# Optimization experiments

Measured on AMD Instinct MI355X. Metric: run time of the kernel, lower is better.

The kernel has to match this reference:

```python
import jax, jax.numpy as jnp
import numpy as np
from jax import lax

# module constants (match init_kwargs)
CHUNK_LENGTH = 32
RIGHT_CONTEXT_LENGTH = 8
CHANNELS = 512
KERNEL_SIZE = 31
CACHE_SIZE = KERNEL_SIZE - 1  # 30


def _conv1d(x, w, b, groups=1):
    # x: (N, C_in, L), w: (C_out, C_in/groups, K), b: (C_out,)
    y = lax.conv_general_dilated(
        x, w, window_strides=(1,), padding='VALID',
        dimension_numbers=('NCH', 'OIH', 'NCH'),
        feature_group_count=groups)
    return y + b[None, :, None]


def setup_inputs() -> dict:
    key = jax.random.key(0)
    ks = jax.random.split(key, 9)
    U, B, D, R = 2048, 16, CHANNELS, 512
    s = 0.02
    return {
        'utterance': jax.random.normal(ks[0], (U, B, D), jnp.float32),
        'right_context': jax.random.normal(ks[1], (R, B, D), jnp.float32),
        'cache': jnp.zeros((B, D, CACHE_SIZE), jnp.float32),
        'w1': jax.random.normal(ks[2], (2 * D, D, 1), jnp.float32) * s,
        'b1': jax.random.normal(ks[3], (2 * D,), jnp.float32) * s,
        'wd': jax.random.normal(ks[4], (D, 1, KERNEL_SIZE), jnp.float32) * s,
        'bd': jax.random.normal(ks[5], (D,), jnp.float32) * s,
        'w2': jax.random.normal(ks[6], (D, D, 1), jnp.float32) * s,
        'b2': jax.random.normal(ks[7], (D,), jnp.float32) * s,
    }


def reference(utterance, right_context, cache, w1, b1, wd, bd, w2, b2):
    U, B, D = utterance.shape
    R = right_context.shape[0]
    rcl, cl, cs = RIGHT_CONTEXT_LENGTH, CHUNK_LENGTH, CACHE_SIZE

    # concat [right_context; utterance] along time, to (B, D, R+U)
    x = jnp.concatenate([right_context, utterance], axis=0).transpose(1, 2, 0)
    # pointwise_conv1 (ScaledConv1d == plain conv in forward math) + GLU
    # (ActivationBalancer is identity in forward)
    x = _conv1d(x, w1, b1)  # (B, 2D, R+U)
    a, g = jnp.split(x, 2, axis=1)
    x = a * jax.nn.sigmoid(g)  # GLU -> (B, D, R+U)

    utt = x[:, :, R:]      # (B, D, U)
    rc = x[:, :, :R]       # (B, D, R)

    # causal depthwise conv with left cache
    pad_utt = jnp.concatenate([cache, utt], axis=2)  # (B, D, cs+U)
    new_cache = pad_utt[:, :, -cs:]
    utt = _conv1d(pad_utt, wd, bd, groups=D)  # (B, D, U)

    # _split_right_context: gather per-chunk left cache for each rc segment
    U_ = cs + U
    num_chunks = R // rcl
    pad_utt_t = pad_utt.transpose(2, 0, 1)   # (U_, B, D)
    rc_t = rc.transpose(2, 0, 1)             # (R, B, D)
    end_idx = jnp.minimum(U_, cs + (jnp.arange(num_chunks) + 1) * cl)
    start_idx = end_idx - cs                 # (num_chunks,)
    gidx = start_idx[:, None] + jnp.arange(cs)[None, :]   # (nc, cs)
    padding = pad_utt_t[gidx]                # (nc, cs, B, D)
    padding = padding.transpose(0, 2, 1, 3).reshape(num_chunks * B, cs, D)
    rc_seg = rc_t.reshape(num_chunks, rcl, B, D).transpose(0, 2, 1, 3)
    rc_seg = rc_seg.reshape(num_chunks * B, rcl, D)
    pad_rc = jnp.concatenate([padding, rc_seg], axis=1).transpose(0, 2, 1)  # (nc*B, D, cs+rcl)
    rc_out = _conv1d(pad_rc, wd, bd, groups=D)  # (nc*B, D, rcl)
    # _merge_right_context
    rc_out = rc_out.reshape(num_chunks, B, D, rcl).transpose(1, 2, 0, 3)
    rc_out = rc_out.reshape(B, D, R)

    x = jnp.concatenate([rc_out, utt], axis=2)  # (B, D, R+U)
    # DoubleSwish: x * sigmoid(x - 1)
    x = x * jax.nn.sigmoid(x - 1.0)
    x = _conv1d(x, w2, b2)  # pointwise_conv2

    rc_final = x[:, :, :R].transpose(2, 0, 1)   # (R, B, D)
    utt_final = x[:, :, R:].transpose(2, 0, 1)  # (U, B, D)
    return utt_final, rc_final, new_cache
```

## Files before the change

### kernel.cpp

```cpp
#include <hip/hip_runtime.h>
#include <math.h>

#define B_SZ 16
#define D_CH 512
#define U_LEN 2048
#define R_LEN 512
#define T_LEN 2560
#define KS 31
#define CS 30

typedef __attribute__((ext_vector_type(8))) short short8;
typedef __attribute__((ext_vector_type(4))) float floatx4;

__device__ __forceinline__ float bf2f(ushort u) {
    unsigned v = (unsigned)u << 16;
    float f; __builtin_memcpy(&f, &v, 4); return f;
}
__device__ __forceinline__ ushort f2bf(float f) {
    unsigned v; __builtin_memcpy(&v, &f, 4);
    v += 0x7fff + ((v >> 16) & 1);
    return (ushort)(v >> 16);
}
__device__ __forceinline__ float sigmoidf_(float x) { return 1.0f / (1.0f + __expf(-x)); }

__device__ __forceinline__ void gld16(const void* g, void* l) {
    __builtin_amdgcn_global_load_lds((const __attribute__((address_space(1))) void*)g,
                                     (__attribute__((address_space(3))) void*)l, 16, 0, 0);
}

__global__ __launch_bounds__(256) void k_conv_all(
    const float* __restrict__ utt, const float* __restrict__ rc, const float* __restrict__ cache,
    const float* __restrict__ w1, const float* __restrict__ w2,
    ushort* __restrict__ xb, ushort* __restrict__ w1b, ushort* __restrict__ w2b,
    ushort* __restrict__ xc)
{
    int blk = blockIdx.x;
    if (blk < 5120) {
        size_t f4 = (size_t)blk * 1024 + threadIdx.x * 4;
        size_t o = f4 * 4;
        int q = (int)(o >> 9), d = (int)(o & 511);
        const float* src = (q < 8192) ? rc + ((size_t)q << 9) + d
                                      : utt + (((size_t)(q - 8192)) << 9) + d;
        ushort* dst = xb + o;
        #pragma unroll
        for (int i = 0; i < 4; ++i) {
            float4 v = ((const float4*)src)[i];
            ushort4 u4; u4.x = f2bf(v.x); u4.y = f2bf(v.y); u4.z = f2bf(v.z); u4.w = f2bf(v.w);
            ((ushort4*)dst)[i] = u4;
        }
    } else if (blk < 5312) {
        int t = (blk - 5120) * 1024 + threadIdx.x * 4;
        const float* src; ushort* dst;
        if (t < 131072) { src = w1; dst = w1b; }
        else            { t -= 131072; src = w2; dst = w2b; }
        #pragma unroll
        for (int i = 0; i < 4; ++i) {
            float4 v = ((const float4*)src)[t + i];
            ushort4 u4; u4.x = f2bf(v.x); u4.y = f2bf(v.y); u4.z = f2bf(v.z); u4.w = f2bf(v.w);
            ((ushort4*)dst)[t + i] = u4;
        }
    } else {
        int o = (blk - 5312) * 256 + threadIdx.x;
        int d = o & 511, p = o >> 13, b = (o >> 9) & 15;
        xc[o] = f2bf(cache[((size_t)b * D_CH + d) * CS + p]);
    }
}

__global__ __launch_bounds__(256) void k1_mfma(
    const ushort* __restrict__ xb, const ushort* __restrict__ w1b,
    const float* __restrict__ b1, ushort* __restrict__ y)
{
    __shared__ __attribute__((aligned(16))) ushort sA[2][256 * 32];
    __shared__ __attribute__((aligned(16))) ushort sBa[2][64 * 32];
    __shared__ __attribute__((aligned(16))) ushort sBg[2][64 * 32];
    const int tid = threadIdx.x;
    const int w = tid >> 6, lane = tid & 63;
    const int f = blockIdx.x;
    const int xcd = f & 7, nn = (f >> 3) & 7, qh = f >> 6;
    const int q0 = (qh * 8 + xcd) * 256;
    const int n0 = nn * 64;
    const int col = lane & 15, quad = lane >> 4;

    floatx4 acc_a[4][4], acc_g[4][4];
    #pragma unroll
    for (int i = 0; i < 4; ++i)
        #pragma unroll
        for (int j = 0; j < 4; ++j) { acc_a[i][j] = 0.f; acc_g[i][j] = 0.f; }

    const int sBs = w * 64 + lane;
    const int sBr = sBs >> 2, sBh = sBs & 3;

#define STAGE1(kc, buf) do { \
        _Pragma("unroll") \
        for (int jj = 0; jj < 4; ++jj) { \
            int s = (w * 4 + jj) * 64 + lane; \
            gld16(xb + (((size_t)(q0 + (s >> 2))) << 9) + (kc) + (s & 3) * 8, \
                  &sA[buf][(w * 4 + jj) * 512]); \
        } \
        gld16(w1b + (((size_t)(n0 + sBr)) << 9) + (kc) + sBh * 8, &sBa[buf][w * 512]); \
        gld16(w1b + (((size_t)(512 + n0 + sBr)) << 9) + (kc) + sBh * 8, &sBg[buf][w * 512]); \
    } while (0)

    STAGE1(0, 0);
    #pragma unroll
    for (int kc = 0; kc < 512; kc += 32) {
        const int buf = (kc >> 5) & 1;
        __syncthreads();
        if (kc + 32 < 512) STAGE1(kc + 32, buf ^ 1);

        short8 af[4], ba[4], bg[4];
        #pragma unroll
        for (int i = 0; i < 4; ++i)
            af[i] = *(const short8*)&sA[buf][(w * 64 + i * 16 + col) * 32 + quad * 8];
        #pragma unroll
        for (int j = 0; j < 4; ++j) {
            ba[j] = *(const short8*)&sBa[buf][(j * 16 + col) * 32 + quad * 8];
            bg[j] = *(const short8*)&sBg[buf][(j * 16 + col) * 32 + quad * 8];
        }
        #pragma unroll
        for (int i = 0; i < 4; ++i)
            #pragma unroll
            for (int j = 0; j < 4; ++j) {
                acc_a[i][j] = __builtin_amdgcn_mfma_f32_16x16x32_bf16(af[i], ba[j], acc_a[i][j], 0, 0, 0);
                acc_g[i][j] = __builtin_amdgcn_mfma_f32_16x16x32_bf16(af[i], bg[j], acc_g[i][j], 0, 0, 0);
            }
    }
#undef STAGE1

    #pragma unroll
    for (int j = 0; j < 4; ++j) {
        float bia = b1[n0 + j * 16 + col];
        float big = b1[512 + n0 + j * 16 + col];
        #pragma unroll
        for (int i = 0; i < 4; ++i) {
            #pragma unroll
            for (int r = 0; r < 4; ++r) {
                int row = q0 + w * 64 + i * 16 + quad * 4 + r;
                float a = acc_a[i][j][r] + bia;
                float g = acc_g[i][j][r] + big;
                y[((size_t)row << 9) + n0 + j * 16 + col] = f2bf(a * sigmoidf_(g));
            }
        }
    }
}

__global__ __launch_bounds__(256) void k2_fused(
    const ushort* __restrict__ y, const ushort* __restrict__ xc,
    const float* __restrict__ wd, const float* __restrict__ bd,
    ushort* __restrict__ z, float* __restrict__ out)
{
    __shared__ __attribute__((aligned(16))) char smem[20352];
    const int tid = threadIdx.x;
    int g = blockIdx.x;

    if (g < 4096) {
        ushort* sy = (ushort*)smem;
        float*  sw = (float*)(smem + 12416);
        const int u0 = (g & 31) * 64;
        const int d0 = ((g >> 5) & 7) * 64;
        const int b  = g >> 8;

        for (int idx = tid; idx < 94 * 8; idx += 256) {
            int r  = idx >> 3;
            int c8 = idx & 7;
            int p  = u0 + r;
            int dg = d0 + c8 * 8;
            const ushort* src = (p < CS) ? xc + (((size_t)(p * 16 + b)) << 9) + dg
                                         : y  + (((size_t)((482 + p) * 16 + b)) << 9) + dg;
            ushort tmp[8];
            *(int4*)tmp = *(const int4*)src;
            #pragma unroll
            for (int j = 0; j < 8; ++j) sy[(c8 * 8 + j) * 97 + r] = tmp[j];
        }
        for (int idx = tid; idx < 64 * 31; idx += 256) {
            int d = idx / 31, k = idx - d * 31;
            sw[d * 31 + k] = wd[(size_t)(d0 + d) * KS + k];
        }
        __syncthreads();

        const int dl   = tid & 63;
        const int useg = (tid >> 6) * 16;
        float win[46];
        #pragma unroll
        for (int p = 0; p < 46; ++p) win[p] = bf2f(sy[dl * 97 + useg + p]);
        float bias = bd[d0 + dl];
        float acc[16];
        #pragma unroll
        for (int i = 0; i < 16; ++i) acc[i] = bias;
        for (int k = 0; k < 31; ++k) {
            float w = sw[dl * 31 + k];
            #pragma unroll
            for (int i = 0; i < 16; ++i) acc[i] = fmaf(w, win[k + i], acc[i]);
        }
        #pragma unroll
        for (int i = 0; i < 16; ++i) {
            float v = acc[i];
            v = v * sigmoidf_(v - 1.0f);
            int u = u0 + useg + i;
            z[(((size_t)((R_LEN + u) * 16 + b)) << 9) + d0 + dl] = f2bf(v);
        }
        if ((g & 31) == 31) {
            for (int idx = tid; idx < 64 * 30; idx += 256) {
                int dl2 = idx & 63, j = idx >> 6;
                out[(size_t)20971520 + ((size_t)b * D_CH + d0 + dl2) * CS + j] = bf2f(sy[dl2 * 97 + 64 + j]);
            }
        }
    } else {
        g -= 4096;
        ushort* sy = (ushort*)smem;
        const int i  = g & 63;
        const int b  = (g >> 6) & 15;
        const int dbase = (g >> 10) * 256;

        for (int idx = tid; idx < 38 * 32; idx += 256) {
            int r  = idx >> 5;
            int c8 = idx & 31;
            int t = (r < CS) ? (R_LEN + 32 * i + 2 + r) : (8 * i + (r - CS));
            *(int4*)&sy[r * 256 + c8 * 8] =
                *(const int4*)(y + (((size_t)(t * 16 + b)) << 9) + dbase + c8 * 8);
        }
        __syncthreads();

        const int dd = dbase + tid;
        float wr[31];
        #pragma unroll
        for (int k = 0; k < 31; ++k) wr[k] = wd[(size_t)dd * KS + k];
        float bias = bd[dd];
        #pragma unroll
        for (int j = 0; j < 8; ++j) {
            float acc = bias;
            #pragma unroll
            for (int k = 0; k < 31; ++k) acc = fmaf(wr[k], bf2f(sy[(j + k) * 256 + tid]), acc);
            float v = acc * sigmoidf_(acc - 1.0f);
            z[(((size_t)((i * 8 + j) * 16 + b)) << 9) + dd] = f2bf(v);
        }
    }
}

__global__ __launch_bounds__(256) void k3_mfma(
    const ushort* __restrict__ zb, const ushort* __restrict__ w2b,
    const float* __restrict__ b2, float* __restrict__ out)
{
    __shared__ __attribute__((aligned(16))) ushort sA[2][256 * 32];
    __shared__ __attribute__((aligned(16))) ushort sB[2][64 * 32];
    const int tid = threadIdx.x;
    const int w = tid >> 6, lane = tid & 63;
    const int f = blockIdx.x;
    const int xcd = f & 7, nn = (f >> 3) & 7, qh = f >> 6;
    const int q0 = (qh * 8 + xcd) * 256;
    const int n0 = nn * 64;
    const int col = lane & 15, quad = lane >> 4;

    floatx4 acc[4][4];
    #pragma unroll
    for (int i = 0; i < 4; ++i)
        #pragma unroll
        for (int j = 0; j < 4; ++j) acc[i][j] = 0.f;

    const int sBs = w * 64 + lane;
    const int sBr = sBs >> 2, sBh = sBs & 3;

#define STAGE3(kc, buf) do { \
        _Pragma("unroll") \
        for (int jj = 0; jj < 4; ++jj) { \
            int s = (w * 4 + jj) * 64 + lane; \
            gld16(zb + (((size_t)(q0 + (s >> 2))) << 9) + (kc) + (s & 3) * 8, \
                  &sA[buf][(w * 4 + jj) * 512]); \
        } \
        gld16(w2b + (((size_t)(n0 + sBr)) << 9) + (kc) + sBh * 8, &sB[buf][w * 512]); \
    } while (0)

    STAGE3(0, 0);
    #pragma unroll
    for (int kc = 0; kc < 512; kc += 32) {
        const int buf = (kc >> 5) & 1;
        __syncthreads();
        if (kc + 32 < 512) STAGE3(kc + 32, buf ^ 1);

        short8 af[4], bf[4];
        #pragma unroll
        for (int i = 0; i < 4; ++i)
            af[i] = *(const short8*)&sA[buf][(w * 64 + i * 16 + col) * 32 + quad * 8];
        #pragma unroll
        for (int j = 0; j < 4; ++j)
            bf[j] = *(const short8*)&sB[buf][(j * 16 + col) * 32 + quad * 8];
        #pragma unroll
        for (int i = 0; i < 4; ++i)
            #pragma unroll
            for (int j = 0; j < 4; ++j)
                acc[i][j] = __builtin_amdgcn_mfma_f32_16x16x32_bf16(af[i], bf[j], acc[i][j], 0, 0, 0);
    }
#undef STAGE3

    #pragma unroll
    for (int j = 0; j < 4; ++j) {
        float bb = b2[n0 + j * 16 + col];
        #pragma unroll
        for (int i = 0; i < 4; ++i) {
            #pragma unroll
            for (int r = 0; r < 4; ++r) {
                int q = q0 + w * 64 + i * 16 + quad * 4 + r;
                float v = acc[i][j][r] + bb;
                size_t off = (q < 8192) ? (size_t)16777216 + ((size_t)q << 9)
                                        : ((size_t)(q - 8192) << 9);
                out[off + n0 + j * 16 + col] = v;
            }
        }
    }
}

extern "C" void kernel_launch(void* const* d_in, const int* in_sizes, int n_in,
                              void* d_out, int out_size, void* d_ws, size_t ws_size,
                              hipStream_t stream)
{
    const float* utt   = (const float*)d_in[0];
    const float* rc    = (const float*)d_in[1];
    const float* cache = (const float*)d_in[2];
    const float* w1    = (const float*)d_in[3];
    const float* b1    = (const float*)d_in[4];
    const float* wd    = (const float*)d_in[5];
    const float* bd    = (const float*)d_in[6];
    const float* w2    = (const float*)d_in[7];
    const float* b2    = (const float*)d_in[8];
    float* out = (float*)d_out;

    ushort* xb  = (ushort*)d_ws;
    ushort* y   = xb  + (size_t)20971520;
    ushort* zb  = y   + (size_t)20971520;
    ushort* w1b = zb  + (size_t)20971520;
    ushort* w2b = w1b + (size_t)524288;
    ushort* xc  = w2b + (size_t)262144;

    k_conv_all<<<dim3(6272), 256, 0, stream>>>(utt, rc, cache, w1, w2, xb, w1b, w2b, xc);
    k1_mfma   <<<dim3(1280), 256, 0, stream>>>(xb, w1b, b1, y);
    k2_fused  <<<dim3(6144), 256, 0, stream>>>(y, xc, wd, bd, zb, out);
    k3_mfma   <<<dim3(1280), 256, 0, stream>>>(zb, w2b, b2, out);
}
```

Before: 354.1 us.

## Retile pointwise GEMMs to 128x128 with 4-stage swizzled LDS pipeline

Both MFMA GEMM kernels switch from a 256x64 tile to a 128x128 tile with a 2x2 wave layout. LDS goes from double to quad buffering, with manual vmcnt waits and an XOR swizzle to avoid bank conflicts. MFMA sections run at raised wave priority. For the first GEMM, the w1 rows are interleaved at conversion time so each 16-column fragment pair holds matching GLU value and gate columns, letting one accumulator set cover both and letting the epilogue pair them. The aim is better operand reuse, deeper latency hiding and two blocks per CU, at the cost of relying on hand-written wait counts.

```diff
diff --git a/kernel.cpp b/kernel.cpp
--- a/kernel.cpp
+++ b/kernel.cpp
@@ -50,14 +50,25 @@
         }
     } else if (blk < 5312) {
         int t = (blk - 5120) * 1024 + threadIdx.x * 4;
-        const float* src; ushort* dst;
-        if (t < 131072) { src = w1; dst = w1b; }
-        else            { t -= 131072; src = w2; dst = w2b; }
-        #pragma unroll
-        for (int i = 0; i < 4; ++i) {
-            float4 v = ((const float4*)src)[t + i];
-            ushort4 u4; u4.x = f2bf(v.x); u4.y = f2bf(v.y); u4.z = f2bf(v.z); u4.w = f2bf(v.w);
-            ((ushort4*)dst)[t + i] = u4;
+        if (t < 131072) {
+            #pragma unroll
+            for (int i = 0; i < 4; ++i) {
+                int e = (t + i) << 2;
+                int row = e >> 9, k = e & 511;
+                int rr = row & 511;
+                int rp = (rr >> 4) * 32 + ((row >> 9) << 4) + (rr & 15);
+                float4 v = ((const float4*)w1)[t + i];
+                ushort4 u4; u4.x = f2bf(v.x); u4.y = f2bf(v.y); u4.z = f2bf(v.z); u4.w = f2bf(v.w);
+                ((ushort4*)w1b)[rp * 128 + (k >> 2)] = u4;
+            }
+        } else {
+            int t2 = t - 131072;
+            #pragma unroll
+            for (int i = 0; i < 4; ++i) {
+                float4 v = ((const float4*)w2)[t2 + i];
+                ushort4 u4; u4.x = f2bf(v.x); u4.y = f2bf(v.y); u4.z = f2bf(v.z); u4.w = f2bf(v.w);
+                ((ushort4*)w2b)[t2 + i] = u4;
+            }
         }
     } else {
         int o = (blk - 5312) * 256 + threadIdx.x;
@@ -66,79 +77,88 @@
     }
 }
 
-__global__ __launch_bounds__(256) void k1_mfma(
-    const ushort* __restrict__ xb, const ushort* __restrict__ w1b,
+__global__ __launch_bounds__(256, 2) void k1_mfma(
+    const ushort* __restrict__ xb, const ushort* __restrict__ w1p,
     const float* __restrict__ b1, ushort* __restrict__ y)
 {
-    __shared__ __attribute__((aligned(16))) ushort sA[2][256 * 32];
-    __shared__ __attribute__((aligned(16))) ushort sBa[2][64 * 32];
-    __shared__ __attribute__((aligned(16))) ushort sBg[2][64 * 32];
+    __shared__ __attribute__((aligned(16))) ushort lds[4][2][4096];
     const int tid = threadIdx.x;
     const int w = tid >> 6, lane = tid & 63;
-    const int f = blockIdx.x;
-    const int xcd = f & 7, nn = (f >> 3) & 7, qh = f >> 6;
-    const int q0 = (qh * 8 + xcd) * 256;
-    const int n0 = nn * 64;
     const int col = lane & 15, quad = lane >> 4;
-
-    floatx4 acc_a[4][4], acc_g[4][4];
+    const int wm = w >> 1, wn = w & 1;
+    const int bid = blockIdx.x;
+    const int f = (bid & 7) * 320 + (bid >> 3);
+    const int mt = f >> 3, nn = f & 7;
+    const int q0 = mt * 128, n0 = nn * 128;
+
+    floatx4 acc[4][4];
     #pragma unroll
     for (int i = 0; i < 4; ++i)
         #pragma unroll
-        for (int j = 0; j < 4; ++j) { acc_a[i][j] = 0.f; acc_g[i][j] = 0.f; }
-
-    const int sBs = w * 64 + lane;
-    const int sBr = sBs >> 2, sBh = sBs & 3;
-
-#define STAGE1(kc, buf) do { \
-        _Pragma("unroll") \
-        for (int jj = 0; jj < 4; ++jj) { \
-            int s = (w * 4 + jj) * 64 + lane; \
-            gld16(xb + (((size_t)(q0 + (s >> 2))) << 9) + (kc) + (s & 3) * 8, \
-                  &sA[buf][(w * 4 + jj) * 512]); \
-        } \
-        gld16(w1b + (((size_t)(n0 + sBr)) << 9) + (kc) + sBh * 8, &sBa[buf][w * 512]); \
-        gld16(w1b + (((size_t)(512 + n0 + sBr)) << 9) + (kc) + sBh * 8, &sBg[buf][w * 512]); \
+        for (int j = 0; j < 4; ++j) acc[i][j] = 0.f;
+
+    int offA[4], offB[4];
+    #pragma unroll
+    for (int i = 0; i < 4; ++i) {
+        int rA = wm * 64 + i * 16 + col;
+        offA[i] = rA * 64 + ((quad ^ ((rA >> 1) & 3)) << 4);
+        int rB = wn * 64 + i * 16 + col;
+        offB[i] = rB * 64 + ((quad ^ ((rB >> 1) & 3)) << 4);
+    }
+
+    const int srow = tid >> 2;
+    const int sqs = (tid & 3) ^ ((srow >> 1) & 3);
+    const ushort* gA0 = xb  + (((size_t)(q0 + srow))      << 9) + (sqs << 3);
+    const ushort* gA1 = xb  + (((size_t)(q0 + 64 + srow)) << 9) + (sqs << 3);
+    const ushort* gB0 = w1p + (((size_t)(n0 + srow))      << 9) + (sqs << 3);
+    const ushort* gB1 = w1p + (((size_t)(n0 + 64 + srow)) << 9) + (sqs << 3);
+
+#define STAGE1(t_, bi_) do { \
+        const int kc_ = (t_) << 5; \
+        gld16(gA0 + kc_, &lds[bi_][0][w * 512]); \
+        gld16(gA1 + kc_, &lds[bi_][0][2048 + w * 512]); \
+        gld16(gB0 + kc_, &lds[bi_][1][w * 512]); \
+        gld16(gB1 + kc_, &lds[bi_][1][2048 + w * 512]); \
     } while (0)
 
-    STAGE1(0, 0);
-    #pragma unroll
-    for (int kc = 0; kc < 512; kc += 32) {
-        const int buf = (kc >> 5) & 1;
-        __syncthreads();
-        if (kc + 32 < 512) STAGE1(kc + 32, buf ^ 1);
-
-        short8 af[4], ba[4], bg[4];
+    STAGE1(0, 0); STAGE1(1, 1); STAGE1(2, 2);
+
+    #pragma unroll
+    for (int s = 0; s < 16; ++s) {
+        if (s < 14)       asm volatile("s_waitcnt vmcnt(8)\n\ts_barrier" ::: "memory");
+        else if (s == 14) asm volatile("s_waitcnt vmcnt(4)\n\ts_barrier" ::: "memory");
+        else              asm volatile("s_waitcnt vmcnt(0)\n\ts_barrier" ::: "memory");
+        if (s < 13) STAGE1(s + 3, (s + 3) & 3);
+        const char* A  = (const char*)&lds[s & 3][0][0];
+        const char* Bp = (const char*)&lds[s & 3][1][0];
+        short8 af[4], bf8[4];
+        #pragma unroll
+        for (int i = 0; i < 4; ++i) af[i]  = *(const short8*)(A + offA[i]);
+        #pragma unroll
+        for (int j = 0; j < 4; ++j) bf8[j] = *(const short8*)(Bp + offB[j]);
+        __builtin_amdgcn_s_setprio(1);
         #pragma unroll
         for (int i = 0; i < 4; ++i)
-            af[i] = *(const short8*)&sA[buf][(w * 64 + i * 16 + col) * 32 + quad * 8];
-        #pragma unroll
-        for (int j = 0; j < 4; ++j) {
-            ba[j] = *(const short8*)&sBa[buf][(j * 16 + col) * 32 + quad * 8];
-            bg[j] = *(const short8*)&sBg[buf][(j * 16 + col) * 32 + quad * 8];
-        }
-        #pragma unroll
-        for (int i = 0; i < 4; ++i)
-            #pragma unroll
-            for (int j = 0; j < 4; ++j) {
-                acc_a[i][j] = __builtin_amdgcn_mfma_f32_16x16x32_bf16(af[i], ba[j], acc_a[i][j], 0, 0, 0);
-                acc_g[i][j] = __builtin_amdgcn_mfma_f32_16x16x32_bf16(af[i], bg[j], acc_g[i][j], 0, 0, 0);
-            }
+            #pragma unroll
+            for (int j = 0; j < 4; ++j)
+                acc[i][j] = __builtin_amdgcn_mfma_f32_16x16x32_bf16(af[i], bf8[j], acc[i][j], 0, 0, 0);
+        __builtin_amdgcn_s_setprio(0);
     }
 #undef STAGE1
 
-    #pragma unroll
-    for (int j = 0; j < 4; ++j) {
-        float bia = b1[n0 + j * 16 + col];
-        float big = b1[512 + n0 + j * 16 + col];
+    const int nb2 = (n0 + wn * 64) >> 1;
+    #pragma unroll
+    for (int fe = 0; fe < 2; ++fe) {
+        const int na = nb2 + fe * 16 + col;
+        const float ba = b1[na], bg = b1[512 + na];
         #pragma unroll
         for (int i = 0; i < 4; ++i) {
+            const int row = q0 + wm * 64 + i * 16 + quad * 4;
             #pragma unroll
             for (int r = 0; r < 4; ++r) {
-                int row = q0 + w * 64 + i * 16 + quad * 4 + r;
-                float a = acc_a[i][j][r] + bia;
-                float g = acc_g[i][j][r] + big;
-                y[((size_t)row << 9) + n0 + j * 16 + col] = f2bf(a * sigmoidf_(g));
+                float a = acc[i][2 * fe][r] + ba;
+                float g = acc[i][2 * fe + 1][r] + bg;
+                y[(((size_t)(row + r)) << 9) + na] = f2bf(a * sigmoidf_(g));
             }
         }
     }
@@ -237,19 +257,19 @@
     }
 }
 
-__global__ __launch_bounds__(256) void k3_mfma(
+__global__ __launch_bounds__(256, 2) void k3_mfma(
     const ushort* __restrict__ zb, const ushort* __restrict__ w2b,
     const float* __restrict__ b2, float* __restrict__ out)
 {
-    __shared__ __attribute__((aligned(16))) ushort sA[2][256 * 32];
-    __shared__ __attribute__((aligned(16))) ushort sB[2][64 * 32];
+    __shared__ __attribute__((aligned(16))) ushort lds[4][2][4096];
     const int tid = threadIdx.x;
     const int w = tid >> 6, lane = tid & 63;
-    const int f = blockIdx.x;
-    const int xcd = f & 7, nn = (f >> 3) & 7, qh = f >> 6;
-    const int q0 = (qh * 8 + xcd) * 256;
-    const int n0 = nn * 64;
     const int col = lane & 15, quad = lane >> 4;
+    const int wm = w >> 1, wn = w & 1;
+    const int bid = blockIdx.x;
+    const int f = (bid & 7) * 160 + (bid >> 3);
+    const int mt = f >> 2, nn = f & 3;
+    const int q0 = mt * 128, n0 = nn * 128;
 
     floatx4 acc[4][4];
     #pragma unroll
@@ -257,53 +277,69 @@
         #pragma unroll
         for (int j = 0; j < 4; ++j) acc[i][j] = 0.f;
 
-    const int sBs = w * 64 + lane;
-    const int sBr = sBs >> 2, sBh = sBs & 3;
-
-#define STAGE3(kc, buf) do { \
-        _Pragma("unroll") \
-        for (int jj = 0; jj < 4; ++jj) { \
-            int s = (w * 4 + jj) * 64 + lane; \
-            gld16(zb + (((size_t)(q0 + (s >> 2))) << 9) + (kc) + (s & 3) * 8, \
-                  &sA[buf][(w * 4 + jj) * 512]); \
-        } \
-        gld16(w2b + (((size_t)(n0 + sBr)) << 9) + (kc) + sBh * 8, &sB[buf][w * 512]); \
+    int offA[4], offB[4];
+    #pragma unroll
+    for (int i = 0; i < 4; ++i) {
+        int rA = wm * 64 + i * 16 + col;
+        offA[i] = rA * 64 + ((quad ^ ((rA >> 1) & 3)) << 4);
+        int rB = wn * 64 + i * 16 + col;
+        offB[i] = rB * 64 + ((quad ^ ((rB >> 1) & 3)) << 4);
+    }
+
+    const int srow = tid >> 2;
+    const int sqs = (tid & 3) ^ ((srow >> 1) & 3);
+    const ushort* gA0 = zb  + (((size_t)(q0 + srow))      << 9) + (sqs << 3);
+    const ushort* gA1 = zb  + (((size_t)(q0 + 64 + srow)) << 9) + (sqs << 3);
+    const ushort* gB0 = w2b + (((size_t)(n0 + srow))      << 9) + (sqs << 3);
+    const ushort* gB1 = w2b + (((size_t)(n0 + 64 + srow)) << 9) + (sqs << 3);
+
+#define STAGE3(t_, bi_) do { \
+        const int kc_ = (t_) << 5; \
+        gld16(gA0 + kc_, &lds[bi_][0][w * 512]); \
+        gld16(gA1 + kc_, &lds[bi_][0][2048 + w * 512]); \
+        gld16(gB0 + kc_, &lds[bi_][1][w * 512]); \
+        gld16(gB1 + kc_, &lds[bi_][1][2048 + w * 512]); \
     } while (0)
 
-    STAGE3(0, 0);
-    #pragma unroll
-    for (int kc = 0; kc < 512; kc += 32) {
-        const int buf = (kc >> 5) & 1;
-        __syncthreads();
-        if (kc + 32 < 512) STAGE3(kc + 32, buf ^ 1);
-
-        short8 af[4], bf[4];
+    STAGE3(0, 0); STAGE3(1, 1); STAGE3(2, 2);
+
+    #pragma unroll
+    for (int s = 0; s < 16; ++s) {
+        if (s < 14)       asm volatile("s_waitcnt vmcnt(8)\n\ts_barrier" ::: "memory");
+        else if (s == 14) asm volatile("s_waitcnt vmcnt(4)\n\ts_barrier" ::: "memory");
+        else              asm volatile("s_waitcnt vmcnt(0)\n\ts_barrier" ::: "memory");
+        if (s < 13) STAGE3(s + 3, (s + 3) & 3);
+        const char* A  = (const char*)&lds[s & 3][0][0];
+        const char* Bp = (const char*)&lds[s & 3][1][0];
+        short8 af[4], bf8[4];
+        #pragma unroll
+        for (int i = 0; i < 4; ++i) af[i]  = *(const short8*)(A + offA[i]);
+        #pragma unroll
+        for (int j = 0; j < 4; ++j) bf8[j] = *(const short8*)(Bp + offB[j]);
+        __builtin_amdgcn_s_setprio(1);
         #pragma unroll
         for (int i = 0; i < 4; ++i)
-            af[i] = *(const short8*)&sA[buf][(w * 64 + i * 16 + col) * 32 + quad * 8];
-        #pragma unroll
-        for (int j = 0; j < 4; ++j)
-            bf[j] = *(const short8*)&sB[buf][(j * 16 + col) * 32 + quad * 8];
-        #pragma unroll
-        for (int i = 0; i < 4; ++i)
             #pragma unroll
             for (int j = 0; j < 4; ++j)
-                acc[i][j] = __builtin_amdgcn_mfma_f32_16x16x32_bf16(af[i], bf[j], acc[i][j], 0, 0, 0);
+                acc[i][j] = __builtin_amdgcn_mfma_f32_16x16x32_bf16(af[i], bf8[j], acc[i][j], 0, 0, 0);
+        __builtin_amdgcn_s_setprio(0);
     }
 #undef STAGE3
 
     #pragma unroll
     for (int j = 0; j < 4; ++j) {
-        float bb = b2[n0 + j * 16 + col];
+        const int n = n0 + wn * 64 + j * 16 + col;
+        const float bb = b2[n];
         #pragma unroll
         for (int i = 0; i < 4; ++i) {
+            const int qrow = q0 + wm * 64 + i * 16 + quad * 4;
             #pragma unroll
             for (int r = 0; r < 4; ++r) {
-                int q = q0 + w * 64 + i * 16 + quad * 4 + r;
+                const int q = qrow + r;
                 float v = acc[i][j][r] + bb;
                 size_t off = (q < 8192) ? (size_t)16777216 + ((size_t)q << 9)
                                         : ((size_t)(q - 8192) << 9);
-                out[off + n0 + j * 16 + col] = v;
+                out[off + n] = v;
             }
         }
     }
@@ -332,7 +368,7 @@
     ushort* xc  = w2b + (size_t)262144;
 
     k_conv_all<<<dim3(6272), 256, 0, stream>>>(utt, rc, cache, w1, w2, xb, w1b, w2b, xc);
-    k1_mfma   <<<dim3(1280), 256, 0, stream>>>(xb, w1b, b1, y);
+    k1_mfma   <<<dim3(2560), 256, 0, stream>>>(xb, w1b, b1, y);
     k2_fused  <<<dim3(6144), 256, 0, stream>>>(y, xc, wd, bd, zb, out);
     k3_mfma   <<<dim3(1280), 256, 0, stream>>>(zb, w2b, b2, out);
 }
```

Result: faster. 309.3 us (-12.7%).
